# Performance work log

Hardware: AMD Instinct MI355X
Metric: run time of the kernel (lower is better)

## Reference

```python
import jax, jax.numpy as jnp
from jax import lax
import numpy as np

B, S, T, I, H, O = 128, 144, 50, 10, 64, 1


def setup_inputs() -> dict:
    key = jax.random.key(0)
    ks = jax.random.split(key, 11)
    sI = 1.0 / np.sqrt(H)
    x = jax.random.normal(ks[0], (B, S, T, I), dtype=jnp.float32)
    # PyTorch nn.GRU weights per direction: W_ih [3H,I], W_hh [3H,H], b_ih [3H], b_hh [3H]
    Wih_f = jax.random.normal(ks[1], (T, 3 * H, I), dtype=jnp.float32) * sI
    Whh_f = jax.random.normal(ks[2], (T, 3 * H, H), dtype=jnp.float32) * sI
    bih_f = jax.random.normal(ks[3], (T, 3 * H), dtype=jnp.float32) * sI
    bhh_f = jax.random.normal(ks[4], (T, 3 * H), dtype=jnp.float32) * sI
    Wih_b = jax.random.normal(ks[5], (T, 3 * H, I), dtype=jnp.float32) * sI
    Whh_b = jax.random.normal(ks[6], (T, 3 * H, H), dtype=jnp.float32) * sI
    bih_b = jax.random.normal(ks[7], (T, 3 * H), dtype=jnp.float32) * sI
    bhh_b = jax.random.normal(ks[8], (T, 3 * H), dtype=jnp.float32) * sI
    Wfc = jax.random.normal(ks[9], (T, O, 2 * H), dtype=jnp.float32) * sI
    bfc = jax.random.normal(ks[10], (T, O), dtype=jnp.float32) * sI
    return {"x": x, "Wih_f": Wih_f, "Whh_f": Whh_f, "bih_f": bih_f, "bhh_f": bhh_f,
            "Wih_b": Wih_b, "Whh_b": Whh_b, "bih_b": bih_b, "bhh_b": bhh_b,
            "Wfc": Wfc, "bfc": bfc}


def _gru_cell(x_t, h, Wih, Whh, bih, bhh):
    # PyTorch GRU cell math
    gi = x_t @ Wih.T + bih          # [B, 3H]
    gh = h @ Whh.T + bhh            # [B, 3H]
    i_r, i_z, i_n = jnp.split(gi, 3, axis=-1)
    h_r, h_z, h_n = jnp.split(gh, 3, axis=-1)
    r = jax.nn.sigmoid(i_r + h_r)
    z = jax.nn.sigmoid(i_z + h_z)
    n = jnp.tanh(i_n + r * h_n)
    return (1.0 - z) * n + z * h


def _per_turbine(xt, wih_f, whh_f, bih_f, bhh_f, wih_b, whh_b, bih_b, bhh_b, wfc, bfc):
    # xt: [B, S, I]
    x_sbi = jnp.transpose(xt, (1, 0, 2))  # [S, B, I]
    h0 = jnp.zeros((xt.shape[0], H), xt.dtype)

    def step(h, x_t):
        h = _gru_cell(x_t, h, wih_f, whh_f, bih_f, bhh_f)
        return h, None

    hf, _ = lax.scan(step, h0, x_sbi)  # forward final hidden = fwd output at t=S-1
    # backward-direction output at last timestep = first step of the reverse scan
    hb = _gru_cell(xt[:, -1, :], h0, wih_b, whh_b, bih_b, bhh_b)
    h = jnp.concatenate([hf, hb], axis=-1)  # [B, 2H]; dropout is identity at inference
    return h @ wfc.T + bfc  # [B, O]


def reference(x, Wih_f, Whh_f, bih_f, bhh_f, Wih_b, Whh_b, bih_b, bhh_b, Wfc, bfc):
    x_tbsi = jnp.transpose(x, (2, 0, 1, 3))  # [T, B, S, I]
    out = jax.vmap(_per_turbine)(x_tbsi, Wih_f, Whh_f, bih_f, bhh_f,
                                 Wih_b, Whh_b, bih_b, bhh_b, Wfc, bfc)  # [T, B, O]
    return jnp.transpose(out, (1, 2, 0))  # [B, O, T]
```

## Files before the change

kernel.cpp:

```cpp
#include <hip/hip_runtime.h>


typedef _Float16 f16;
typedef _Float16 f16x8 __attribute__((ext_vector_type(8)));
typedef float    f32x4 __attribute__((ext_vector_type(4)));

constexpr int B_N = 128, S_N = 144, T_N = 50, I_N = 10, H_N = 64, G3 = 192;
constexpr int BT = 16, NB = B_N / BT;
constexpr int HST = 88;

#define MFMA16(a, b, c) __builtin_amdgcn_mfma_f32_16x16x32_f16((a), (b), (c), 0, 0, 0)

__device__ __forceinline__ float fsig(float v) {
    return __builtin_amdgcn_rcpf(1.0f + __builtin_amdgcn_exp2f(-1.44269504089f * v));
}
__device__ __forceinline__ float ftanh(float v) {
    return 1.0f - 2.0f * __builtin_amdgcn_rcpf(1.0f + __builtin_amdgcn_exp2f(2.88539008178f * v));
}


#define LOADX(ss, q0, q1, q2, q3, q4)                                             \
    if ((ss) < S_N) {                                                             \
        const float* _p = x + (((size_t)(b0 + lc) * S_N + (ss)) * T_N + t) * I_N; \
        if (lg == 0) {                                                            \
            q0 = *(const float2*)(_p);     q1 = *(const float2*)(_p + 2);         \
            q2 = *(const float2*)(_p + 4); q3 = *(const float2*)(_p + 6);         \
        } else if (lg == 1) {                                                     \
            q4 = *(const float2*)(_p + 8);                                        \
        }                                                                         \
    }

#define STEP(ss, q0, q1, q2, q3, q4)                                              \
    {                                                                             \
        const int cur = (ss) & 1, nxt = cur ^ 1;                                  \
        const f16* hrow = &hL[cur][lc][0];                                        \
        const f16x8 hA0 = *(const f16x8*)(hrow + lg * 8);                         \
        const f16x8 hA1 = *(const f16x8*)(hrow + 32 + lg * 8);                    \
        f16x8 xA;                                                                 \
        _Pragma("unroll")                                                         \
        for (int e = 0; e < 8; ++e) xA[e] = (f16)0.0f;                            \
        if (lg == 0) {                                                            \
            xA[0] = (f16)q0.x; xA[1] = (f16)q0.y; xA[2] = (f16)q1.x; xA[3] = (f16)q1.y; \
            xA[4] = (f16)q2.x; xA[5] = (f16)q2.y; xA[6] = (f16)q3.x; xA[7] = (f16)q3.y; \
        } else if (lg == 1) {                                                     \
            xA[0] = (f16)q4.x; xA[1] = (f16)q4.y; xA[2] = (f16)1.0f;              \
        }                                                                         \
        LOADX((ss) + 2, q0, q1, q2, q3, q4)                                       \
        f32x4 aR  = {0.f, 0.f, 0.f, 0.f};                                         \
        f32x4 aZ  = {0.f, 0.f, 0.f, 0.f};                                         \
        f32x4 aNH = {0.f, 0.f, 0.f, 0.f};                                         \
        f32x4 aNX = {0.f, 0.f, 0.f, 0.f};                                         \
        aR  = MFMA16(xA,  BxR,  aR);                                              \
        aZ  = MFMA16(xA,  BxZ,  aZ);                                              \
        aNX = MFMA16(xA,  BxN,  aNX);                                             \
        aR  = MFMA16(hA0, BhR0, aR);                                              \
        aR  = MFMA16(hA1, BhR1, aR);                                              \
        aZ  = MFMA16(hA0, BhZ0, aZ);                                              \
        aZ  = MFMA16(hA1, BhZ1, aZ);                                              \
        aNH = MFMA16(hA0, BhN0, aNH);                                             \
        aNH = MFMA16(hA1, BhN1, aNH);                                             \
        const int r0 = lg * 4;                                                    \
        {                                                                         \
            const float rr = fsig(aR[0]), zz = fsig(aZ[0]);                       \
            const float nn = ftanh(aNX[0] + rr * (aNH[0] + bnh));                 \
            ho0 = nn + zz * (ho0 - nn);                                           \
            hL[nxt][r0 + 0][uc + lc] = (f16)ho0;                                  \
        }                                                                         \
        {                                                                         \
            const float rr = fsig(aR[1]), zz = fsig(aZ[1]);                       \
            const float nn = ftanh(aNX[1] + rr * (aNH[1] + bnh));                 \
            ho1 = nn + zz * (ho1 - nn);                                           \
            hL[nxt][r0 + 1][uc + lc] = (f16)ho1;                                  \
        }                                                                         \
        {                                                                         \
            const float rr = fsig(aR[2]), zz = fsig(aZ[2]);                       \
            const float nn = ftanh(aNX[2] + rr * (aNH[2] + bnh));                 \
            ho2 = nn + zz * (ho2 - nn);                                           \
            hL[nxt][r0 + 2][uc + lc] = (f16)ho2;                                  \
        }                                                                         \
        {                                                                         \
            const float rr = fsig(aR[3]), zz = fsig(aZ[3]);                       \
            const float nn = ftanh(aNX[3] + rr * (aNH[3] + bnh));                 \
            ho3 = nn + zz * (ho3 - nn);                                           \
            hL[nxt][r0 + 3][uc + lc] = (f16)ho3;                                  \
        }                                                                         \
        __syncthreads();                                                          \
    }

__global__ __launch_bounds__(256, 2)
void gru_mfma(const float* __restrict__ x,
              const float* __restrict__ Wih_f, const float* __restrict__ Whh_f,
              const float* __restrict__ bih_f, const float* __restrict__ bhh_f,
              const float* __restrict__ Wih_b, const float* __restrict__ bih_b,
              const float* __restrict__ bhh_b,
              const float* __restrict__ Wfc,   const float* __restrict__ bfc,
              float* __restrict__ out)
{
    __shared__ f16   hL[2][BT][HST];
    __shared__ float hfL[BT][H_N + 1];
    __shared__ float hbL[BT][H_N + 1];

    const int tid = threadIdx.x;
    const int w   = tid >> 6, l = tid & 63;
    const int uc  = w * 16;
    const int lc  = l & 15;
    const int lg  = l >> 4;
    const int t   = blockIdx.x / NB;
    const int b0  = (blockIdx.x % NB) * BT;

    {
        f16* hp = &hL[0][0][0];
        for (int i = tid; i < BT * HST; i += 256) hp[i] = (f16)0.0f;
    }

    const float* Whh = Whh_f + (size_t)t * G3 * H_N;
    const float* Wih = Wih_f + (size_t)t * G3 * I_N;

    auto loadBh = [&](int g, int kk) -> f16x8 {
        const float4* p = (const float4*)(Whh + (size_t)g * H_N + kk * 32 + lg * 8);
        const float4 a = p[0], b = p[1];
        f16x8 v;
        v[0] = (f16)a.x; v[1] = (f16)a.y; v[2] = (f16)a.z; v[3] = (f16)a.w;
        v[4] = (f16)b.x; v[5] = (f16)b.y; v[6] = (f16)b.z; v[7] = (f16)b.w;
        return v;
    };
    auto loadBx = [&](int g, bool rz) -> f16x8 {
        f16x8 v;
        #pragma unroll
        for (int j = 0; j < 8; ++j) {
            const int k = lg * 8 + j;
            float val = 0.0f;
            if (k < I_N)       val = Wih[(size_t)g * I_N + k];
            else if (k == 10)  val = bih_f[t * G3 + g] + (rz ? bhh_f[t * G3 + g] : 0.0f);
            v[j] = (f16)val;
        }
        return v;
    };

    const f16x8 BhR0 = loadBh(uc + lc, 0),       BhR1 = loadBh(uc + lc, 1);
    const f16x8 BhZ0 = loadBh(64 + uc + lc, 0),  BhZ1 = loadBh(64 + uc + lc, 1);
    const f16x8 BhN0 = loadBh(128 + uc + lc, 0), BhN1 = loadBh(128 + uc + lc, 1);
    const f16x8 BxR  = loadBx(uc + lc, true);
    const f16x8 BxZ  = loadBx(64 + uc + lc, true);
    const f16x8 BxN  = loadBx(128 + uc + lc, false);
    const float bnh  = bhh_f[t * G3 + 128 + uc + lc];

    float2 xa0 = {0.f,0.f}, xa1 = {0.f,0.f}, xa2 = {0.f,0.f}, xa3 = {0.f,0.f}, xa4 = {0.f,0.f};
    float2 xb0 = {0.f,0.f}, xb1 = {0.f,0.f}, xb2 = {0.f,0.f}, xb3 = {0.f,0.f}, xb4 = {0.f,0.f};
    LOADX(0, xa0, xa1, xa2, xa3, xa4)
    LOADX(1, xb0, xb1, xb2, xb3, xb4)

    float ho0 = 0.f, ho1 = 0.f, ho2 = 0.f, ho3 = 0.f;

    __syncthreads();

    for (int s = 0; s < S_N; s += 2) {
        STEP(s,     xa0, xa1, xa2, xa3, xa4)
        STEP(s + 1, xb0, xb1, xb2, xb3, xb4)
    }

    {
        const int r0 = lg * 4;
        hfL[r0 + 0][uc + lc] = ho0;
        hfL[r0 + 1][uc + lc] = ho1;
        hfL[r0 + 2][uc + lc] = ho2;
        hfL[r0 + 3][uc + lc] = ho3;
    }

    {
        const int row2 = tid >> 4;
        const int j0   = (tid & 15) * 4;
        const float* wib = Wih_b + (size_t)t * G3 * I_N;
        const float* bib = bih_b + t * G3;
        const float* bhb = bhh_b + t * G3;
        float xr[I_N];
        #pragma unroll
        for (int k = 0; k < I_N; ++k)
            xr[k] = x[(((size_t)(b0 + row2) * S_N + (S_N - 1)) * T_N + t) * I_N + k];
        #pragma unroll
        for (int m = 0; m < 4; ++m) {
            const int j = j0 + m;
            float ir = bib[j], iz = bib[64 + j], inn = bib[128 + j];
            #pragma unroll
            for (int k = 0; k < I_N; ++k) {
                const float xv = xr[k];
                ir  += wib[(size_t)j * I_N + k]          * xv;
                iz  += wib[(size_t)(64 + j) * I_N + k]   * xv;
                inn += wib[(size_t)(128 + j) * I_N + k]  * xv;
            }
            const float r  = fsig(ir + bhb[j]);
            const float z  = fsig(iz + bhb[64 + j]);
            const float nn = ftanh(inn + r * bhb[128 + j]);
            hbL[row2][j] = (1.0f - z) * nn;
        }
    }
    __syncthreads();

    if (tid < BT) {
        const float* wfc = Wfc + (size_t)t * 2 * H_N;
        float acc = bfc[t];
        #pragma unroll 4
        for (int j = 0; j < H_N; ++j) acc += hfL[tid][j] * wfc[j];
        #pragma unroll 4
        for (int j = 0; j < H_N; ++j) acc += hbL[tid][j] * wfc[64 + j];
        out[(size_t)(b0 + tid) * T_N + t] = acc;
    }
}

extern "C" void kernel_launch(void* const* d_in, const int* in_sizes, int n_in,
                              void* d_out, int out_size, void* d_ws, size_t ws_size,
                              hipStream_t stream) {
    const float* x     = (const float*)d_in[0];
    const float* Wih_f = (const float*)d_in[1];
    const float* Whh_f = (const float*)d_in[2];
    const float* bih_f = (const float*)d_in[3];
    const float* bhh_f = (const float*)d_in[4];
    const float* Wih_b = (const float*)d_in[5];
    const float* bih_b = (const float*)d_in[7];
    const float* bhh_b = (const float*)d_in[8];
    const float* Wfc   = (const float*)d_in[9];
    const float* bfc   = (const float*)d_in[10];
    float* out = (float*)d_out;

    dim3 grid(T_N * NB), block(256);
    hipLaunchKernelGGL(gru_mfma, grid, block, 0, stream,
                       x, Wih_f, Whh_f, bih_f, bhh_f, Wih_b, bih_b, bhh_b, Wfc, bfc, out);
}
```

Measured before the change: 118.9 us.

## Pre-pack x to padded fp16, fold exp2 scales into weights, lighten barrier

Adds a pre-pass kernel that converts x into padded 16-element fp16 rows with a bias-one column, so the recurrent loop does one vector load per step instead of several float2 loads and per-element conversions. The log2(e) and sign scalings for the sigmoid and tanh are folded into the fp16 weights, so the gate math feeds exp2 directly without extra multiplies. __syncthreads is replaced by an explicit lgkmcnt wait plus s_barrier. The cost is an extra kernel launch and a workspace write and read of the packed x, plus some fp16 rounding from scaling the weights before conversion. The packed path runs only when the workspace is large enough.

Result: faster. 102.4 us (-13.8%).

```diff
diff --git a/kernel.cpp b/kernel.cpp
--- a/kernel.cpp
+++ b/kernel.cpp
@@ -8,18 +8,37 @@
 constexpr int B_N = 128, S_N = 144, T_N = 50, I_N = 10, H_N = 64, G3 = 192;
 constexpr int BT = 16, NB = B_N / BT;
 constexpr int HST = 88;
+constexpr float L2E = 1.44269504089f;
 
 #define MFMA16(a, b, c) __builtin_amdgcn_mfma_f32_16x16x32_f16((a), (b), (c), 0, 0, 0)
 
 __device__ __forceinline__ float fsig(float v) {
-    return __builtin_amdgcn_rcpf(1.0f + __builtin_amdgcn_exp2f(-1.44269504089f * v));
+    return __builtin_amdgcn_rcpf(1.0f + __builtin_amdgcn_exp2f(-L2E * v));
 }
 __device__ __forceinline__ float ftanh(float v) {
-    return 1.0f - 2.0f * __builtin_amdgcn_rcpf(1.0f + __builtin_amdgcn_exp2f(2.88539008178f * v));
-}
-
-
-#define LOADX(ss, q0, q1, q2, q3, q4)                                             \
+    return 1.0f - 2.0f * __builtin_amdgcn_rcpf(1.0f + __builtin_amdgcn_exp2f(2.0f * L2E * v));
+}
+
+__global__ __launch_bounds__(256)
+void pack_x(const float* __restrict__ x, f16* __restrict__ xP) {
+    const int idx = blockIdx.x * 256 + threadIdx.x;
+    if (idx >= B_N * S_N * T_N) return;
+    const float* s = x + (size_t)idx * I_N;
+    f16x8 lo, hi;
+    #pragma unroll
+    for (int e = 0; e < 8; ++e) lo[e] = (f16)s[e];
+    hi[0] = (f16)s[8]; hi[1] = (f16)s[9]; hi[2] = (f16)1.0f;
+    #pragma unroll
+    for (int e = 3; e < 8; ++e) hi[e] = (f16)0.0f;
+    f16* d = xP + (size_t)idx * 16;
+    *(f16x8*)d = lo; *(f16x8*)(d + 8) = hi;
+}
+
+#define LOADX_P(ss, xf)                                                           \
+    if ((ss) < S_N && lg < 2)                                                     \
+        xf = *(const f16x8*)(xProw + (size_t)(ss) * (T_N * 16) + lg * 8);
+
+#define LOADX_R(ss, q0, q1, q2, q3, q4)                                           \
     if ((ss) < S_N) {                                                             \
         const float* _p = x + (((size_t)(b0 + lc) * S_N + (ss)) * T_N + t) * I_N; \
         if (lg == 0) {                                                            \
@@ -30,22 +49,27 @@
         }                                                                         \
     }
 
-#define STEP(ss, q0, q1, q2, q3, q4)                                              \
+#define STEP(ss, xf, q0, q1, q2, q3, q4)                                          \
     {                                                                             \
         const int cur = (ss) & 1, nxt = cur ^ 1;                                  \
         const f16* hrow = &hL[cur][lc][0];                                        \
         const f16x8 hA0 = *(const f16x8*)(hrow + lg * 8);                         \
         const f16x8 hA1 = *(const f16x8*)(hrow + 32 + lg * 8);                    \
         f16x8 xA;                                                                 \
-        _Pragma("unroll")                                                         \
-        for (int e = 0; e < 8; ++e) xA[e] = (f16)0.0f;                            \
-        if (lg == 0) {                                                            \
-            xA[0] = (f16)q0.x; xA[1] = (f16)q0.y; xA[2] = (f16)q1.x; xA[3] = (f16)q1.y; \
-            xA[4] = (f16)q2.x; xA[5] = (f16)q2.y; xA[6] = (f16)q3.x; xA[7] = (f16)q3.y; \
-        } else if (lg == 1) {                                                     \
-            xA[0] = (f16)q4.x; xA[1] = (f16)q4.y; xA[2] = (f16)1.0f;              \
+        if constexpr (PX) {                                                       \
+            xA = xf;                                                              \
+            LOADX_P((ss) + 2, xf)                                                 \
+        } else {                                                                  \
+            _Pragma("unroll")                                                     \
+            for (int e = 0; e < 8; ++e) xA[e] = (f16)0.0f;                        \
+            if (lg == 0) {                                                        \
+                xA[0] = (f16)q0.x; xA[1] = (f16)q0.y; xA[2] = (f16)q1.x; xA[3] = (f16)q1.y; \
+                xA[4] = (f16)q2.x; xA[5] = (f16)q2.y; xA[6] = (f16)q3.x; xA[7] = (f16)q3.y; \
+            } else if (lg == 1) {                                                 \
+                xA[0] = (f16)q4.x; xA[1] = (f16)q4.y; xA[2] = (f16)1.0f;          \
+            }                                                                     \
+            LOADX_R((ss) + 2, q0, q1, q2, q3, q4)                                 \
         }                                                                         \
-        LOADX((ss) + 2, q0, q1, q2, q3, q4)                                       \
         f32x4 aR  = {0.f, 0.f, 0.f, 0.f};                                         \
         f32x4 aZ  = {0.f, 0.f, 0.f, 0.f};                                         \
         f32x4 aNH = {0.f, 0.f, 0.f, 0.f};                                         \
@@ -60,35 +84,23 @@
         aNH = MFMA16(hA0, BhN0, aNH);                                             \
         aNH = MFMA16(hA1, BhN1, aNH);                                             \
         const int r0 = lg * 4;                                                    \
-        {                                                                         \
-            const float rr = fsig(aR[0]), zz = fsig(aZ[0]);                       \
-            const float nn = ftanh(aNX[0] + rr * (aNH[0] + bnh));                 \
-            ho0 = nn + zz * (ho0 - nn);                                           \
-            hL[nxt][r0 + 0][uc + lc] = (f16)ho0;                                  \
+        _Pragma("unroll")                                                         \
+        for (int j = 0; j < 4; ++j) {                                             \
+            const float rr = __builtin_amdgcn_rcpf(1.0f + __builtin_amdgcn_exp2f(aR[j])); \
+            const float zz = __builtin_amdgcn_rcpf(1.0f + __builtin_amdgcn_exp2f(aZ[j])); \
+            const float qq = __builtin_amdgcn_rcpf(1.0f + __builtin_amdgcn_exp2f(fmaf(rr, aNH[j] + bnhs, aNX[j]))); \
+            const float nn = fmaf(-2.0f, qq, 1.0f);                               \
+            ho[j] = fmaf(zz, ho[j] - nn, nn);                                     \
+            hL[nxt][r0 + j][uc + lc] = (f16)ho[j];                                \
         }                                                                         \
-        {                                                                         \
-            const float rr = fsig(aR[1]), zz = fsig(aZ[1]);                       \
-            const float nn = ftanh(aNX[1] + rr * (aNH[1] + bnh));                 \
-            ho1 = nn + zz * (ho1 - nn);                                           \
-            hL[nxt][r0 + 1][uc + lc] = (f16)ho1;                                  \
-        }                                                                         \
-        {                                                                         \
-            const float rr = fsig(aR[2]), zz = fsig(aZ[2]);                       \
-            const float nn = ftanh(aNX[2] + rr * (aNH[2] + bnh));                 \
-            ho2 = nn + zz * (ho2 - nn);                                           \
-            hL[nxt][r0 + 2][uc + lc] = (f16)ho2;                                  \
-        }                                                                         \
-        {                                                                         \
-            const float rr = fsig(aR[3]), zz = fsig(aZ[3]);                       \
-            const float nn = ftanh(aNX[3] + rr * (aNH[3] + bnh));                 \
-            ho3 = nn + zz * (ho3 - nn);                                           \
-            hL[nxt][r0 + 3][uc + lc] = (f16)ho3;                                  \
-        }                                                                         \
-        __syncthreads();                                                          \
-    }
-
+        asm volatile("s_waitcnt lgkmcnt(0)" ::: "memory");                        \
+        __builtin_amdgcn_s_barrier();                                             \
+        asm volatile("" ::: "memory");                                            \
+    }
+
+template<bool PX>
 __global__ __launch_bounds__(256, 2)
-void gru_mfma(const float* __restrict__ x,
+void gru_mfma(const float* __restrict__ x, const f16* __restrict__ xP,
               const float* __restrict__ Wih_f, const float* __restrict__ Whh_f,
               const float* __restrict__ bih_f, const float* __restrict__ bhh_f,
               const float* __restrict__ Wih_b, const float* __restrict__ bih_b,
@@ -115,16 +127,18 @@
 
     const float* Whh = Whh_f + (size_t)t * G3 * H_N;
     const float* Wih = Wih_f + (size_t)t * G3 * I_N;
-
-    auto loadBh = [&](int g, int kk) -> f16x8 {
+    const f16*  xProw = PX ? (xP + ((size_t)(b0 + lc) * S_N * T_N + t) * 16) : nullptr;
+
+    const float sRZ = -L2E, sN = 2.0f * L2E;
+    auto loadBh = [&](int g, int kk, float sc) -> f16x8 {
         const float4* p = (const float4*)(Whh + (size_t)g * H_N + kk * 32 + lg * 8);
         const float4 a = p[0], b = p[1];
         f16x8 v;
-        v[0] = (f16)a.x; v[1] = (f16)a.y; v[2] = (f16)a.z; v[3] = (f16)a.w;
-        v[4] = (f16)b.x; v[5] = (f16)b.y; v[6] = (f16)b.z; v[7] = (f16)b.w;
+        v[0] = (f16)(sc * a.x); v[1] = (f16)(sc * a.y); v[2] = (f16)(sc * a.z); v[3] = (f16)(sc * a.w);
+        v[4] = (f16)(sc * b.x); v[5] = (f16)(sc * b.y); v[6] = (f16)(sc * b.z); v[7] = (f16)(sc * b.w);
         return v;
     };
-    auto loadBx = [&](int g, bool rz) -> f16x8 {
+    auto loadBx = [&](int g, bool rz, float sc) -> f16x8 {
         f16x8 v;
         #pragma unroll
         for (int j = 0; j < 8; ++j) {
@@ -132,39 +146,47 @@
             float val = 0.0f;
             if (k < I_N)       val = Wih[(size_t)g * I_N + k];
             else if (k == 10)  val = bih_f[t * G3 + g] + (rz ? bhh_f[t * G3 + g] : 0.0f);
-            v[j] = (f16)val;
+            v[j] = (f16)(sc * val);
         }
         return v;
     };
 
-    const f16x8 BhR0 = loadBh(uc + lc, 0),       BhR1 = loadBh(uc + lc, 1);
-    const f16x8 BhZ0 = loadBh(64 + uc + lc, 0),  BhZ1 = loadBh(64 + uc + lc, 1);
-    const f16x8 BhN0 = loadBh(128 + uc + lc, 0), BhN1 = loadBh(128 + uc + lc, 1);
-    const f16x8 BxR  = loadBx(uc + lc, true);
-    const f16x8 BxZ  = loadBx(64 + uc + lc, true);
-    const f16x8 BxN  = loadBx(128 + uc + lc, false);
-    const float bnh  = bhh_f[t * G3 + 128 + uc + lc];
-
-    float2 xa0 = {0.f,0.f}, xa1 = {0.f,0.f}, xa2 = {0.f,0.f}, xa3 = {0.f,0.f}, xa4 = {0.f,0.f};
-    float2 xb0 = {0.f,0.f}, xb1 = {0.f,0.f}, xb2 = {0.f,0.f}, xb3 = {0.f,0.f}, xb4 = {0.f,0.f};
-    LOADX(0, xa0, xa1, xa2, xa3, xa4)
-    LOADX(1, xb0, xb1, xb2, xb3, xb4)
-
-    float ho0 = 0.f, ho1 = 0.f, ho2 = 0.f, ho3 = 0.f;
+    const f16x8 BhR0 = loadBh(uc + lc, 0, sRZ),        BhR1 = loadBh(uc + lc, 1, sRZ);
+    const f16x8 BhZ0 = loadBh(64 + uc + lc, 0, sRZ),   BhZ1 = loadBh(64 + uc + lc, 1, sRZ);
+    const f16x8 BhN0 = loadBh(128 + uc + lc, 0, sN),   BhN1 = loadBh(128 + uc + lc, 1, sN);
+    const f16x8 BxR  = loadBx(uc + lc, true, sRZ);
+    const f16x8 BxZ  = loadBx(64 + uc + lc, true, sRZ);
+    const f16x8 BxN  = loadBx(128 + uc + lc, false, sN);
+    const float bnhs = sN * bhh_f[t * G3 + 128 + uc + lc];
+
+    f16x8 xpA, xpB;
+    #pragma unroll
+    for (int e = 0; e < 8; ++e) { xpA[e] = (f16)0.0f; xpB[e] = (f16)0.0f; }
+    float2 ra0 = {0.f,0.f}, ra1 = {0.f,0.f}, ra2 = {0.f,0.f}, ra3 = {0.f,0.f}, ra4 = {0.f,0.f};
+    float2 rb0 = {0.f,0.f}, rb1 = {0.f,0.f}, rb2 = {0.f,0.f}, rb3 = {0.f,0.f}, rb4 = {0.f,0.f};
+    if constexpr (PX) {
+        LOADX_P(0, xpA)
+        LOADX_P(1, xpB)
+    } else {
+        LOADX_R(0, ra0, ra1, ra2, ra3, ra4)
+        LOADX_R(1, rb0, rb1, rb2, rb3, rb4)
+    }
+
+    float ho[4] = {0.f, 0.f, 0.f, 0.f};
 
     __syncthreads();
 
     for (int s = 0; s < S_N; s += 2) {
-        STEP(s,     xa0, xa1, xa2, xa3, xa4)
-        STEP(s + 1, xb0, xb1, xb2, xb3, xb4)
+        STEP(s,     xpA, ra0, ra1, ra2, ra3, ra4)
+        STEP(s + 1, xpB, rb0, rb1, rb2, rb3, rb4)
     }
 
     {
         const int r0 = lg * 4;
-        hfL[r0 + 0][uc + lc] = ho0;
-        hfL[r0 + 1][uc + lc] = ho1;
-        hfL[r0 + 2][uc + lc] = ho2;
-        hfL[r0 + 3][uc + lc] = ho3;
+        hfL[r0 + 0][uc + lc] = ho[0];
+        hfL[r0 + 1][uc + lc] = ho[1];
+        hfL[r0 + 2][uc + lc] = ho[2];
+        hfL[r0 + 3][uc + lc] = ho[3];
     }
 
     {
@@ -222,7 +244,17 @@
     const float* bfc   = (const float*)d_in[10];
     float* out = (float*)d_out;
 
+    const size_t xp_bytes = (size_t)B_N * S_N * T_N * 16 * sizeof(f16);
     dim3 grid(T_N * NB), block(256);
-    hipLaunchKernelGGL(gru_mfma, grid, block, 0, stream,
-                       x, Wih_f, Whh_f, bih_f, bhh_f, Wih_b, bih_b, bhh_b, Wfc, bfc, out);
-}
+
+    if (ws_size >= xp_bytes) {
+        f16* xP = (f16*)d_ws;
+        const int n = B_N * S_N * T_N;
+        hipLaunchKernelGGL(pack_x, dim3((n + 255) / 256), dim3(256), 0, stream, x, xP);
+        hipLaunchKernelGGL((gru_mfma<true>), grid, block, 0, stream,
+                           x, xP, Wih_f, Whh_f, bih_f, bhh_f, Wih_b, bih_b, bhh_b, Wfc, bfc, out);
+    } else {
+        hipLaunchKernelGGL((gru_mfma<false>), grid, block, 0, stream,
+                           x, nullptr, Wih_f, Whh_f, bih_f, bhh_f, Wih_b, bih_b, bhh_b, Wfc, bfc, out);
+    }
+}
```
